# Performance work log

Hardware: AMD Instinct MI355X
Metric: run time of the kernel (lower is better)

## Reference

```python
import jax, jax.numpy as jnp
import numpy as np

V, SMAX, D, H, L, DFF, W = 32000, 1024, 1024, 16, 2, 4096, 256
HD = D // H
EPS = 1e-6


def setup_inputs() -> dict:
    key = jax.random.key(0)
    ks = jax.random.split(key, 20)
    s = lambda k, shape, scale=0.02: jax.random.normal(k, shape, dtype=jnp.float32) * scale
    return {
        "input_ids": jax.random.randint(ks[0], (2, SMAX), 0, V, dtype=jnp.int64),
        "emb": s(ks[1], (V, D)),
        "pos": s(ks[2], (SMAX, D)),
        "norm1_w": jnp.ones((L, D), jnp.float32),
        "norm2_w": jnp.ones((L, D), jnp.float32),
        "wq": s(ks[3], (L, D, D)), "bq": jnp.zeros((L, D), jnp.float32),
        "wk": s(ks[4], (L, D, D)), "bk": jnp.zeros((L, D), jnp.float32),
        "wv": s(ks[5], (L, D, D)), "bv": jnp.zeros((L, D), jnp.float32),
        "wo": s(ks[6], (L, D, D)), "bo": jnp.zeros((L, D), jnp.float32),
        "w1": s(ks[7], (L, D, DFF)), "b1": jnp.zeros((L, DFF), jnp.float32),
        "w2": s(ks[8], (L, DFF, D)), "b2": jnp.zeros((L, D), jnp.float32),
        "normf_w": jnp.ones((D,), jnp.float32),
    }


def rms(x, w):
    return x * jax.lax.rsqrt(jnp.mean(x * x, axis=-1, keepdims=True) + EPS) * w


def reference(input_ids, emb, pos, norm1_w, norm2_w, wq, bq, wk, bk, wv, bv,
              wo, bo, w1, b1, w2, b2, normf_w):
    B, S = input_ids.shape
    x = emb[input_ids] + pos[:S]  # [B,S,D]
    # sliding-window causal mask: attend to j with 0 <= i-j < W
    i = jnp.arange(S)[:, None]
    j = jnp.arange(S)[None, :]
    mask = (j <= i) & (i - j < W)  # [S,S]
    neg = jnp.asarray(-1e9, x.dtype)
    for l in range(L):
        h = rms(x, norm1_w[l])
        q = (h @ wq[l] + bq[l]).reshape(B, S, H, HD)
        k = (h @ wk[l] + bk[l]).reshape(B, S, H, HD)
        v = (h @ wv[l] + bv[l]).reshape(B, S, H, HD)
        scores = jnp.einsum('bqhd,bkhd->bhqk', q, k) / np.sqrt(HD).astype(np.float32)
        scores = jnp.where(mask[None, None], scores, neg)
        attn = jax.nn.softmax(scores, axis=-1)
        o = jnp.einsum('bhqk,bkhd->bqhd', attn, v).reshape(B, S, D)
        x = x + (o @ wo[l] + bo[l])
        h2 = rms(x, norm2_w[l])
        x = x + (jax.nn.gelu(h2 @ w1[l] + b1[l], approximate=False) @ w2[l] + b2[l])
    x = rms(x, normf_w)
    logits = x @ emb.T  # tied lm_head
    return logits
```

## Files before the change

### kernel.cpp

```cpp
#include <hip/hip_runtime.h>
#include <hip/hip_bf16.h>
#include <cstdint>

typedef __bf16 bf16;
typedef __bf16 bf16x8 __attribute__((ext_vector_type(8)));
typedef __bf16 bf16x4 __attribute__((ext_vector_type(4)));
typedef float  f32x4  __attribute__((ext_vector_type(4)));

constexpr int V_    = 32000;
constexpr int SMAX_ = 1024;
constexpr int D_    = 1024;
constexpr int H_    = 16;
constexpr int L_    = 2;
constexpr int DFF_  = 4096;
constexpr int WIN_  = 256;
constexpr int B_    = 2;
constexpr int M_    = B_ * SMAX_;

#define SBAR0_() __builtin_amdgcn_sched_barrier(0)
#define HWBAR_() { __builtin_amdgcn_s_barrier(); SBAR0_(); }
#define LGKM0_() { asm volatile("s_waitcnt lgkmcnt(0)" ::: "memory"); SBAR0_(); }
#define VM0_()   { asm volatile("s_waitcnt vmcnt(0)" ::: "memory"); SBAR0_(); }
#define VM8_()   { asm volatile("s_waitcnt vmcnt(8)" ::: "memory"); SBAR0_(); }

__global__ __launch_bounds__(512, 1) void gemm_lmA(
    const bf16* __restrict__ A, const bf16* __restrict__ BT,
    float* __restrict__ outf, int Nn)
{
  constexpr int KK = 1024, NT = KK / 32;
  __shared__ __align__(16) bf16 ldsA[4 * 8192];
  __shared__ __align__(16) bf16 ldsB[4 * 8192];

  const int t = threadIdx.x, lane = t & 63, w = t >> 6;
  const int l16 = lane & 15, lh = lane >> 4;
  const int wm = w >> 2, wn = w & 3;

  const int nloc = gridDim.x >> 3;
  const int wg = (blockIdx.x & 7) * nloc + (blockIdx.x >> 3);
  const long m0 = (long)(wg & 7) * 256;
  const long n0 = (long)(wg >> 3) * 256;

  auto STG = [&](const bf16* src, long rowBase, bf16* dst, int k0) {
    #pragma unroll
    for (int j = 0; j < 2; ++j) {
      int p = j * 8192 + t * 16;
      int row = p >> 6;
      int sl = ((p >> 4) & 3) ^ (row & 3);
      const bf16* g = src + (rowBase + row) * (long)KK + k0 + sl * 8;
      __builtin_amdgcn_global_load_lds(
          (const __attribute__((address_space(1))) uint32_t*)g,
          (__attribute__((address_space(3))) uint32_t*)(dst + j * 4096 + w * 512),
          16, 0, 0);
    }
  };
  auto LDF = [&](const bf16* base, int rowb) -> bf16x8 {
    int row = rowb + l16;
    return *(const bf16x8*)(base + row * 32 + ((lh ^ (l16 & 3)) << 3));
  };

  f32x4 acc[8][4] = {};

  STG(A, m0, ldsA,          0);  STG(BT, n0, ldsB,          0);
  STG(A, m0, ldsA + 8192,  32);  STG(BT, n0, ldsB + 8192,  32);
  STG(A, m0, ldsA + 16384, 64);  STG(BT, n0, ldsB + 16384, 64);
  int kNext = 96;

  for (int i = 0; i < NT; ++i) {
    const int cur = i & 3, nb = (i + 3) & 3;
    VM8_();
    HWBAR_();
    const bf16* Ac = ldsA + cur * 8192;
    const bf16* Bc = ldsB + cur * 8192;
    bf16x8 af[8], bb[4];
    #pragma unroll
    for (int mi = 0; mi < 8; ++mi) af[mi] = LDF(Ac, wm * 128 + mi * 16);
    #pragma unroll
    for (int ni = 0; ni < 4; ++ni) bb[ni] = LDF(Bc, wn * 64 + ni * 16);
    STG(A, m0, ldsA + nb * 8192, kNext);
    STG(BT, n0, ldsB + nb * 8192, kNext);
    kNext += 32; if (kNext == KK) kNext = 0;
    LGKM0_();
    __builtin_amdgcn_s_setprio(1);
    #pragma unroll
    for (int mi = 0; mi < 8; ++mi)
      #pragma unroll
      for (int ni = 0; ni < 4; ++ni)
        acc[mi][ni] = __builtin_amdgcn_mfma_f32_16x16x32_bf16(bb[ni], af[mi], acc[mi][ni], 0, 0, 0);
    __builtin_amdgcn_s_setprio(0);
  }

  asm volatile("s_waitcnt vmcnt(0) lgkmcnt(0)" ::: "memory");
  #pragma unroll
  for (int mi = 0; mi < 8; ++mi) {
    long row = m0 + wm * 128 + mi * 16 + l16;
    #pragma unroll
    for (int ni = 0; ni < 4; ++ni) {
      long col = n0 + wn * 64 + ni * 16 + lh * 4;
      *(f32x4*)(outf + row * Nn + col) = acc[mi][ni];
    }
  }
}

template<int BM, int EPI>
__global__ __launch_bounds__(256) void gemm_l2(
    const bf16* __restrict__ A, const bf16* __restrict__ BT,
    const float* __restrict__ bias, float* __restrict__ resid,
    bf16* __restrict__ outb, float* __restrict__ outf,
    int Nn, int Kk, int nbyMask, int nbyShift)
{
  constexpr int MR = BM / 32;
  constexpr int CA = BM / 32;
  __shared__ __align__(16) bf16 ldsA[2][BM * 64];
  __shared__ __align__(16) bf16 ldsB[2][8192];

  const int t = threadIdx.x, lane = t & 63, w = t >> 6;
  const int l16 = lane & 15, lh = lane >> 4;
  const int wm = w >> 1, wn = w & 1;

  const int nwg = gridDim.x, bid = blockIdx.x;
  const int nloc = nwg >> 3;
  const int wg = (bid & 7) * nloc + (bid >> 3);
  const long m0 = (long)(wg & nbyMask) * BM;
  const long n0 = (long)(wg >> nbyShift) * 128;

  auto STGA = [&](int c, int k0) {
    #pragma unroll
    for (int q = 0; q < CA; ++q) {
      int row = q * 32 + (t >> 3);
      int sl  = (t & 7) ^ (row & 7);
      const bf16* g = A + (m0 + row) * (long)Kk + k0 + sl * 8;
      __builtin_amdgcn_global_load_lds(
          (const __attribute__((address_space(1))) uint32_t*)g,
          (__attribute__((address_space(3))) uint32_t*)(&ldsA[c][q * 2048 + t * 8]),
          16, 0, 0);
    }
  };
  auto STGB = [&](int c, int k0) {
    #pragma unroll
    for (int q = 0; q < 4; ++q) {
      int row = q * 32 + (t >> 3);
      int sl  = (t & 7) ^ (row & 7);
      const bf16* g = BT + (n0 + row) * (long)Kk + k0 + sl * 8;
      __builtin_amdgcn_global_load_lds(
          (const __attribute__((address_space(1))) uint32_t*)g,
          (__attribute__((address_space(3))) uint32_t*)(&ldsB[c][q * 2048 + t * 8]),
          16, 0, 0);
    }
  };
  auto LDA = [&](int c, int mi, int ks) -> bf16x8 {
    int row = wm * (BM / 2) + mi * 16 + l16;
    int sl  = (ks * 4 + lh) ^ (row & 7);
    return *(const bf16x8*)(&ldsA[c][row * 64 + sl * 8]);
  };
  auto LDB = [&](int c, int ni, int ks) -> bf16x8 {
    int row = wn * 64 + ni * 16 + l16;
    int sl  = (ks * 4 + lh) ^ (row & 7);
    return *(const bf16x8*)(&ldsB[c][row * 64 + sl * 8]);
  };

  f32x4 acc[MR][4] = {};
  bf16x8 a[MR], b[4];

  STGA(0, 0); STGB(0, 0);
  int kNext = 64;

  const int NT = Kk >> 6;
  for (int j = 0; j < NT; ++j) {
    const int c = j & 1;
    VM0_();
    HWBAR_();
    #pragma unroll
    for (int mi = 0; mi < MR; ++mi) a[mi] = LDA(c, mi, 0);
    #pragma unroll
    for (int ni = 0; ni < 4; ++ni) b[ni] = LDB(c, ni, 0);
    STGA(c ^ 1, kNext); STGB(c ^ 1, kNext);
    LGKM0_();
    __builtin_amdgcn_s_setprio(1);
    #pragma unroll
    for (int mi = 0; mi < MR; ++mi)
      #pragma unroll
      for (int ni = 0; ni < 4; ++ni)
        acc[mi][ni] = __builtin_amdgcn_mfma_f32_16x16x32_bf16(b[ni], a[mi], acc[mi][ni], 0, 0, 0);
    __builtin_amdgcn_s_setprio(0);
    HWBAR_();
    #pragma unroll
    for (int mi = 0; mi < MR; ++mi) a[mi] = LDA(c, mi, 1);
    #pragma unroll
    for (int ni = 0; ni < 4; ++ni) b[ni] = LDB(c, ni, 1);
    LGKM0_();
    __builtin_amdgcn_s_setprio(1);
    #pragma unroll
    for (int mi = 0; mi < MR; ++mi)
      #pragma unroll
      for (int ni = 0; ni < 4; ++ni)
        acc[mi][ni] = __builtin_amdgcn_mfma_f32_16x16x32_bf16(b[ni], a[mi], acc[mi][ni], 0, 0, 0);
    __builtin_amdgcn_s_setprio(0);
    kNext += 64; if (kNext == Kk) kNext = 0;
  }

  #pragma unroll
  for (int mi = 0; mi < MR; ++mi) {
    long row = m0 + wm * (BM / 2) + mi * 16 + l16;
    #pragma unroll
    for (int ni = 0; ni < 4; ++ni) {
      long col = n0 + wn * 64 + ni * 16 + lh * 4;
      f32x4 v = acc[mi][ni];
      if (EPI == 3) {
        *(f32x4*)(outf + row * Nn + col) = v;
      } else {
        f32x4 bv = *(const f32x4*)(bias + col);
        v += bv;
        if (EPI == 0) {
          bf16x4 o;
          #pragma unroll
          for (int e = 0; e < 4; ++e) o[e] = (bf16)v[e];
          *(bf16x4*)(outb + row * Nn + col) = o;
        } else if (EPI == 1) {
          bf16x4 o;
          #pragma unroll
          for (int e = 0; e < 4; ++e) {
            float xx = v[e];
            o[e] = (bf16)(0.5f * xx * (1.0f + erff(xx * 0.70710678118654752f)));
          }
          *(bf16x4*)(outb + row * Nn + col) = o;
        } else {
          f32x4 r = *(f32x4*)(resid + row * Nn + col);
          r += v;
          *(f32x4*)(resid + row * Nn + col) = r;
        }
      }
    }
  }
}

__global__ __launch_bounds__(256) void attn_swa(
    const bf16* __restrict__ qkv, bf16* __restrict__ o)
{
  constexpr int PADK = 72;
  constexpr int PADV = 40;
  __shared__ bf16 Qs[64 * PADK];
  __shared__ bf16 Ks[32 * PADK];
  __shared__ bf16 Vt[64 * PADV];
  __shared__ bf16 Ps[4][16 * PADV];

  const int bid = blockIdx.x;
  const int qb = bid & 15;
  const int h  = (bid >> 4) & 15;
  const int b  = bid >> 8;
  const int q0 = qb * 64;
  const int t = threadIdx.x, lane = t & 63, w = t >> 6;
  const int l16 = lane & 15, lh = lane >> 4;

  #pragma unroll
  for (int i = 0; i < 2; i++) {
    int e = t + i * 256;
    int row = e >> 3, cc = e & 7;
    uint4 g = *(const uint4*)(qkv + ((long)(b * SMAX_ + q0 + row)) * 3072 + h * 64 + cc * 8);
    *(uint4*)(Qs + row * PADK + cc * 8) = g;
  }
  __syncthreads();
  bf16x8 aq[2];
  const int qrow = w * 16 + l16;
  #pragma unroll
  for (int ks = 0; ks < 2; ks++)
    aq[ks] = *(const bf16x8*)(Qs + qrow * PADK + ks * 32 + lh * 8);

  float m_run[4], l_run[4];
  f32x4 oacc[4];
  #pragma unroll
  for (int rr = 0; rr < 4; rr++) { m_run[rr] = -1e30f; l_run[rr] = 0.0f; }
  #pragma unroll
  for (int n = 0; n < 4; n++) oacc[n] = (f32x4){0.f, 0.f, 0.f, 0.f};

  const int tlo = q0 - (WIN_ - 1);
  const int jlo = (tlo <= 0) ? 0 : (tlo & ~31);
  const int iq  = q0 + w * 16 + lh * 4;

  for (int j0 = jlo; j0 < q0 + 64; j0 += 32) {
    __syncthreads();
    {
      int row = t >> 3, cc = t & 7;
      long base = ((long)(b * SMAX_ + j0 + row)) * 3072 + h * 64 + cc * 8;
      uint4 gk = *(const uint4*)(qkv + base + 1024);
      *(uint4*)(Ks + row * PADK + cc * 8) = gk;
      bf16x8 vv = *(const bf16x8*)(qkv + base + 2048);
      #pragma unroll
      for (int j = 0; j < 8; j++)
        Vt[(cc * 8 + j) * PADV + row] = vv[j];
    }
    __syncthreads();

    f32x4 s[2] = {(f32x4){0.f,0.f,0.f,0.f}, (f32x4){0.f,0.f,0.f,0.f}};
    #pragma unroll
    for (int nt = 0; nt < 2; nt++)
      #pragma unroll
      for (int ks = 0; ks < 2; ks++) {
        bf16x8 bk = *(const bf16x8*)(Ks + (nt * 16 + l16) * PADK + ks * 32 + lh * 8);
        s[nt] = __builtin_amdgcn_mfma_f32_16x16x32_bf16(aq[ks], bk, s[nt], 0, 0, 0);
      }

    float sc[2][4];
    #pragma unroll
    for (int nt = 0; nt < 2; nt++)
      #pragma unroll
      for (int rr = 0; rr < 4; rr++) {
        int i = iq + rr;
        int j = j0 + nt * 16 + l16;
        float v = s[nt][rr] * 0.125f;
        bool ok = (j <= i) && (i - j < WIN_);
        sc[nt][rr] = ok ? v : -1e30f;
      }

    float pb[2][4], alpha[4];
    #pragma unroll
    for (int rr = 0; rr < 4; rr++) {
      float mt = fmaxf(sc[0][rr], sc[1][rr]);
      #pragma unroll
      for (int off = 1; off < 16; off <<= 1) mt = fmaxf(mt, __shfl_xor(mt, off, 64));
      float mn = fmaxf(m_run[rr], mt);
      float a = __expf(m_run[rr] - mn);
      m_run[rr] = mn; alpha[rr] = a;
      float p0 = __expf(sc[0][rr] - mn);
      float p1 = __expf(sc[1][rr] - mn);
      pb[0][rr] = p0; pb[1][rr] = p1;
      float ls = p0 + p1;
      #pragma unroll
      for (int off = 1; off < 16; off <<= 1) ls += __shfl_xor(ls, off, 64);
      l_run[rr] = l_run[rr] * a + ls;
    }
    #pragma unroll
    for (int n = 0; n < 4; n++)
      #pragma unroll
      for (int rr = 0; rr < 4; rr++) oacc[n][rr] *= alpha[rr];

    #pragma unroll
    for (int rr = 0; rr < 4; rr++) {
      int prow = lh * 4 + rr;
      Ps[w][prow * PADV + l16]      = (bf16)pb[0][rr];
      Ps[w][prow * PADV + 16 + l16] = (bf16)pb[1][rr];
    }
    __syncthreads();

    bf16x8 pa = *(const bf16x8*)(&Ps[w][l16 * PADV + lh * 8]);
    #pragma unroll
    for (int n = 0; n < 4; n++) {
      bf16x8 bv = *(const bf16x8*)(Vt + (n * 16 + l16) * PADV + lh * 8);
      oacc[n] = __builtin_amdgcn_mfma_f32_16x16x32_bf16(pa, bv, oacc[n], 0, 0, 0);
    }
  }

  #pragma unroll
  for (int rr = 0; rr < 4; rr++) {
    int i = iq + rr;
    float inv = 1.0f / l_run[rr];
    #pragma unroll
    for (int n = 0; n < 4; n++)
      o[((long)(b * SMAX_ + i)) * D_ + h * 64 + n * 16 + l16] = (bf16)(oacc[n][rr] * inv);
  }
}

__global__ __launch_bounds__(256) void transpose_cvt(
    const float* __restrict__ src, bf16* __restrict__ dst,
    int Kk, int Nn, long srcL, long dstL)
{
  __shared__ float tile[32][33];
  const int tx = threadIdx.x, ty = threadIdx.y;
  const long n0 = (long)blockIdx.x * 32, k0 = (long)blockIdx.y * 32;
  src += (long)blockIdx.z * srcL;
  dst += (long)blockIdx.z * dstL;
  #pragma unroll
  for (int i = 0; i < 4; i++)
    tile[ty + i * 8][tx] = src[(k0 + ty + i * 8) * Nn + n0 + tx];
  __syncthreads();
  #pragma unroll
  for (int i = 0; i < 4; i++)
    dst[(n0 + ty + i * 8) * Kk + k0 + tx] = (bf16)tile[tx][ty + i * 8];
}

__global__ __launch_bounds__(256) void cvt_bf16(
    const float* __restrict__ src, bf16* __restrict__ dst, long n4)
{
  long i = (long)blockIdx.x * 256 + threadIdx.x;
  if (i >= n4) return;
  float4 v = ((const float4*)src)[i];
  bf16x4 o; o[0] = (bf16)v.x; o[1] = (bf16)v.y; o[2] = (bf16)v.z; o[3] = (bf16)v.w;
  ((bf16x4*)dst)[i] = o;
}

__global__ __launch_bounds__(256) void pack_bqkv(
    const float* __restrict__ bq, const float* __restrict__ bk,
    const float* __restrict__ bv, float* __restrict__ out)
{
  int i = blockIdx.x * 256 + threadIdx.x;
  if (i >= L_ * 3072) return;
  int l = i / 3072, c = i % 3072;
  float v = (c < 1024) ? bq[l * 1024 + c]
          : (c < 2048) ? bk[l * 1024 + c - 1024]
                       : bv[l * 1024 + c - 2048];
  out[i] = v;
}

__global__ __launch_bounds__(256) void embed_k(
    const int* __restrict__ ids, const float* __restrict__ emb,
    const float* __restrict__ pos, float* __restrict__ x)
{
  const int m = blockIdx.x, t = threadIdx.x;
  const int id = ids[m];
  const int s = m & (SMAX_ - 1);
  float4 e = ((const float4*)(emb + (long)id * D_))[t];
  float4 p = ((const float4*)(pos + (long)s * D_))[t];
  float4 rr; rr.x = e.x + p.x; rr.y = e.y + p.y; rr.z = e.z + p.z; rr.w = e.w + p.w;
  ((float4*)(x + (long)m * D_))[t] = rr;
}

__global__ __launch_bounds__(256) void rmsnorm_k(
    const float* __restrict__ x, const float* __restrict__ wgt,
    bf16* __restrict__ out)
{
  __shared__ float red[4];
  const int m = blockIdx.x, t = threadIdx.x;
  float4 v = ((const float4*)(x + (long)m * D_))[t];
  float ss = v.x * v.x + v.y * v.y + v.z * v.z + v.w * v.w;
  #pragma unroll
  for (int off = 1; off < 64; off <<= 1) ss += __shfl_xor(ss, off, 64);
  const int lane = t & 63, w = t >> 6;
  if (lane == 0) red[w] = ss;
  __syncthreads();
  float tot = red[0] + red[1] + red[2] + red[3];
  float rs = rsqrtf(tot * (1.0f / D_) + 1e-6f);
  float4 g = ((const float4*)wgt)[t];
  bf16x4 o;
  o[0] = (bf16)(v.x * rs * g.x); o[1] = (bf16)(v.y * rs * g.y);
  o[2] = (bf16)(v.z * rs * g.z); o[3] = (bf16)(v.w * rs * g.w);
  ((bf16x4*)(out + (long)m * D_))[t] = o;
}

extern "C" void kernel_launch(void* const* d_in, const int* in_sizes, int n_in,
                              void* d_out, int out_size, void* d_ws, size_t ws_size,
                              hipStream_t stream)
{
  const int*   ids = (const int*)d_in[0];
  const float* emb = (const float*)d_in[1];
  const float* pos = (const float*)d_in[2];
  const float* n1w = (const float*)d_in[3];
  const float* n2w = (const float*)d_in[4];
  const float* wq  = (const float*)d_in[5];
  const float* bq  = (const float*)d_in[6];
  const float* wk  = (const float*)d_in[7];
  const float* bk  = (const float*)d_in[8];
  const float* wv  = (const float*)d_in[9];
  const float* bv  = (const float*)d_in[10];
  const float* wo  = (const float*)d_in[11];
  const float* bo  = (const float*)d_in[12];
  const float* w1  = (const float*)d_in[13];
  const float* b1  = (const float*)d_in[14];
  const float* w2  = (const float*)d_in[15];
  const float* b2  = (const float*)d_in[16];
  const float* nfw = (const float*)d_in[17];

  char* p = (char*)d_ws;
  auto alloc = [&](size_t bytes) {
    char* rr = p; p += (bytes + 255) & ~(size_t)255; return rr;
  };
  bf16*  wqkv_t = (bf16*) alloc((size_t)L_ * 3 * 1024 * 1024 * 2);
  bf16*  wo_t   = (bf16*) alloc((size_t)L_ * 1024 * 1024 * 2);
  bf16*  w1_t   = (bf16*) alloc((size_t)L_ * 4096 * 1024 * 2);
  bf16*  w2_t   = (bf16*) alloc((size_t)L_ * 1024 * 4096 * 2);
  bf16*  emb_bf = (bf16*) alloc((size_t)V_ * D_ * 2);
  float* bqkv   = (float*)alloc((size_t)L_ * 3072 * 4);
  float* x      = (float*)alloc((size_t)M_ * D_ * 4);
  bf16*  hbuf   = (bf16*) alloc((size_t)M_ * D_ * 2);
  bf16*  qkv    = (bf16*) alloc((size_t)M_ * 3072 * 2);
  bf16*  obuf   = (bf16*) alloc((size_t)M_ * D_ * 2);
  bf16*  ff     = (bf16*) alloc((size_t)M_ * DFF_ * 2);

  const dim3 b32(32, 8, 1);
  transpose_cvt<<<dim3(32, 32, L_),  b32, 0, stream>>>(wq, wqkv_t,                1024, 1024, 1024 * 1024, 3 * 1024 * 1024);
  transpose_cvt<<<dim3(32, 32, L_),  b32, 0, stream>>>(wk, wqkv_t + 1024 * 1024,  1024, 1024, 1024 * 1024, 3 * 1024 * 1024);
  transpose_cvt<<<dim3(32, 32, L_),  b32, 0, stream>>>(wv, wqkv_t + 2*1024*1024,  1024, 1024, 1024 * 1024, 3 * 1024 * 1024);
  transpose_cvt<<<dim3(32, 32, L_),  b32, 0, stream>>>(wo, wo_t,                  1024, 1024, 1024 * 1024, 1024 * 1024);
  transpose_cvt<<<dim3(128, 32, L_), b32, 0, stream>>>(w1, w1_t,                  1024, 4096, 1024 * 4096, 4096 * 1024);
  transpose_cvt<<<dim3(32, 128, L_), b32, 0, stream>>>(w2, w2_t,                  4096, 1024, 4096 * 1024, 1024 * 4096);
  cvt_bf16<<<32000, 256, 0, stream>>>(emb, emb_bf, (long)V_ * D_ / 4);
  pack_bqkv<<<24, 256, 0, stream>>>(bq, bk, bv, bqkv);
  embed_k<<<M_, 256, 0, stream>>>(ids, emb, pos, x);

  for (int l = 0; l < L_; l++) {
    rmsnorm_k<<<M_, 256, 0, stream>>>(x, n1w + l * D_, hbuf);
    gemm_l2<64, 0><<<dim3(32 * 24), 256, 0, stream>>>(
        hbuf, wqkv_t + (size_t)l * 3 * 1024 * 1024, bqkv + l * 3072,
        nullptr, qkv, nullptr, 3072, 1024, 31, 5);
    attn_swa<<<B_ * H_ * (SMAX_ / 64), 256, 0, stream>>>(qkv, obuf);
    gemm_l2<64, 2><<<dim3(32 * 8), 256, 0, stream>>>(
        obuf, wo_t + (size_t)l * 1024 * 1024, bo + l * D_,
        x, nullptr, nullptr, 1024, 1024, 31, 5);
    rmsnorm_k<<<M_, 256, 0, stream>>>(x, n2w + l * D_, hbuf);
    gemm_l2<128, 1><<<dim3(16 * 32), 256, 0, stream>>>(
        hbuf, w1_t + (size_t)l * 4096 * 1024, b1 + l * DFF_,
        nullptr, ff, nullptr, 4096, 1024, 15, 4);
    gemm_l2<64, 2><<<dim3(32 * 8), 256, 0, stream>>>(
        ff, w2_t + (size_t)l * 1024 * 4096, b2 + l * D_,
        x, nullptr, nullptr, 1024, 4096, 31, 5);
  }
  rmsnorm_k<<<M_, 256, 0, stream>>>(x, nfw, hbuf);
  gemm_lmA<<<dim3(8 * (V_ / 256)), 512, 0, stream>>>(
      hbuf, emb_bf, (float*)d_out, V_);
}
```

Before: 620.6 us.

## Piggyback weight transposes and embedding conversion onto layer-0 kernels as extra blocks

Removes the standalone transpose, convert and bias-pack launches. Their work becomes extra trailing blocks appended to the layer-0 rmsnorm, GEMM and attention launches. Each piece is scheduled one launch ahead of its first consumer, so stream ordering still guarantees correctness. The aim is to fill idle CUs during small or tail-bound kernels and cut launch overhead. In exchange, each host kernel reserves its own LDS footprint for the aux blocks, and the main kernels may be slowed by bandwidth contention.

Result: faster. 558.6 us (-10.0%).

```diff
diff --git a/kernel.cpp b/kernel.cpp
--- a/kernel.cpp
+++ b/kernel.cpp
@@ -23,6 +23,65 @@
 #define VM0_()   { asm volatile("s_waitcnt vmcnt(0)" ::: "memory"); SBAR0_(); }
 #define VM8_()   { asm volatile("s_waitcnt vmcnt(8)" ::: "memory"); SBAR0_(); }
 
+struct AuxArgs {
+  const float *wq, *wk, *wv, *wo, *w1, *w2, *emb, *bq, *bk, *bv;
+  bf16 *wqkv_t, *wo_t, *w1_t, *w2_t, *emb_bf;
+  float *bqkv;
+  int kind;
+  int base;
+};
+
+__device__ __forceinline__ void aux_transpose(
+    const float* src, bf16* dst, int Kk, int Nn, int tid, int t)
+{
+  __shared__ float tile[32][33];
+  const int tx = t & 31, ty = t >> 5;
+  int tilesX = Nn >> 5;
+  int n0 = (tid % tilesX) << 5, k0 = (tid / tilesX) << 5;
+  #pragma unroll
+  for (int i = 0; i < 4; i++)
+    tile[ty + i * 8][tx] = src[(long)(k0 + ty + i * 8) * Nn + n0 + tx];
+  __syncthreads();
+  #pragma unroll
+  for (int i = 0; i < 4; i++)
+    dst[(long)(n0 + ty + i * 8) * Kk + k0 + tx] = (bf16)tile[tx][ty + i * 8];
+}
+
+__device__ __forceinline__ void aux_do(const AuxArgs& A, int b, int t)
+{
+  if (A.kind == 0) {
+    if (b < 8192) {
+      int mat = b >> 11, r = b & 2047, z = r >> 10, tid = r & 1023;
+      const float* s; bf16* d;
+      if (mat == 0)      { s = A.wq + (long)z * 1048576; d = A.wqkv_t + (long)z * 3145728; }
+      else if (mat == 1) { s = A.wk + (long)z * 1048576; d = A.wqkv_t + (long)z * 3145728 + 1048576; }
+      else if (mat == 2) { s = A.wv + (long)z * 1048576; d = A.wqkv_t + (long)z * 3145728 + 2097152; }
+      else               { s = A.wo + (long)z * 1048576; d = A.wo_t   + (long)z * 1048576; }
+      aux_transpose(s, d, 1024, 1024, tid, t);
+    } else {
+      int i = (b - 8192) * 256 + t;
+      if (i < L_ * 3072) {
+        int l = i / 3072, c = i % 3072;
+        float v = (c < 1024) ? A.bq[l * 1024 + c]
+                : (c < 2048) ? A.bk[l * 1024 + c - 1024]
+                             : A.bv[l * 1024 + c - 2048];
+        A.bqkv[i] = v;
+      }
+    }
+  } else if (A.kind == 1) {
+    int z = b >> 12, tid = b & 4095;
+    aux_transpose(A.w1 + (long)z * 4194304, A.w1_t + (long)z * 4194304, 1024, 4096, tid, t);
+  } else if (A.kind == 2) {
+    int z = b >> 12, tid = b & 4095;
+    aux_transpose(A.w2 + (long)z * 4194304, A.w2_t + (long)z * 4194304, 4096, 1024, tid, t);
+  } else if (A.kind == 3) {
+    long i = (long)(A.base + b) * 256 + t;
+    float4 v = ((const float4*)A.emb)[i];
+    bf16x4 o; o[0] = (bf16)v.x; o[1] = (bf16)v.y; o[2] = (bf16)v.z; o[3] = (bf16)v.w;
+    ((bf16x4*)A.emb_bf)[i] = o;
+  }
+}
+
 __global__ __launch_bounds__(512, 1) void gemm_lmA(
     const bf16* __restrict__ A, const bf16* __restrict__ BT,
     float* __restrict__ outf, int Nn)
@@ -106,8 +165,13 @@
     const bf16* __restrict__ A, const bf16* __restrict__ BT,
     const float* __restrict__ bias, float* __restrict__ resid,
     bf16* __restrict__ outb, float* __restrict__ outf,
-    int Nn, int Kk, int nbyMask, int nbyShift)
-{
+    int Nn, int Kk, int nbyMask, int nbyShift,
+    AuxArgs aux, int mainBlocks)
+{
+  if ((int)blockIdx.x >= mainBlocks) {
+    aux_do(aux, (int)blockIdx.x - mainBlocks, threadIdx.x);
+    return;
+  }
   constexpr int MR = BM / 32;
   constexpr int CA = BM / 32;
   __shared__ __align__(16) bf16 ldsA[2][BM * 64];
@@ -117,7 +181,7 @@
   const int l16 = lane & 15, lh = lane >> 4;
   const int wm = w >> 1, wn = w & 1;
 
-  const int nwg = gridDim.x, bid = blockIdx.x;
+  const int nwg = mainBlocks, bid = blockIdx.x;
   const int nloc = nwg >> 3;
   const int wg = (bid & 7) * nloc + (bid >> 3);
   const long m0 = (long)(wg & nbyMask) * BM;
@@ -234,8 +298,13 @@
 }
 
 __global__ __launch_bounds__(256) void attn_swa(
-    const bf16* __restrict__ qkv, bf16* __restrict__ o)
-{
+    const bf16* __restrict__ qkv, bf16* __restrict__ o,
+    AuxArgs aux, int mainBlocks)
+{
+  if ((int)blockIdx.x >= mainBlocks) {
+    aux_do(aux, (int)blockIdx.x - mainBlocks, threadIdx.x);
+    return;
+  }
   constexpr int PADK = 72;
   constexpr int PADV = 40;
   __shared__ bf16 Qs[64 * PADK];
@@ -359,47 +428,6 @@
   }
 }
 
-__global__ __launch_bounds__(256) void transpose_cvt(
-    const float* __restrict__ src, bf16* __restrict__ dst,
-    int Kk, int Nn, long srcL, long dstL)
-{
-  __shared__ float tile[32][33];
-  const int tx = threadIdx.x, ty = threadIdx.y;
-  const long n0 = (long)blockIdx.x * 32, k0 = (long)blockIdx.y * 32;
-  src += (long)blockIdx.z * srcL;
-  dst += (long)blockIdx.z * dstL;
-  #pragma unroll
-  for (int i = 0; i < 4; i++)
-    tile[ty + i * 8][tx] = src[(k0 + ty + i * 8) * Nn + n0 + tx];
-  __syncthreads();
-  #pragma unroll
-  for (int i = 0; i < 4; i++)
-    dst[(n0 + ty + i * 8) * Kk + k0 + tx] = (bf16)tile[tx][ty + i * 8];
-}
-
-__global__ __launch_bounds__(256) void cvt_bf16(
-    const float* __restrict__ src, bf16* __restrict__ dst, long n4)
-{
-  long i = (long)blockIdx.x * 256 + threadIdx.x;
-  if (i >= n4) return;
-  float4 v = ((const float4*)src)[i];
-  bf16x4 o; o[0] = (bf16)v.x; o[1] = (bf16)v.y; o[2] = (bf16)v.z; o[3] = (bf16)v.w;
-  ((bf16x4*)dst)[i] = o;
-}
-
-__global__ __launch_bounds__(256) void pack_bqkv(
-    const float* __restrict__ bq, const float* __restrict__ bk,
-    const float* __restrict__ bv, float* __restrict__ out)
-{
-  int i = blockIdx.x * 256 + threadIdx.x;
-  if (i >= L_ * 3072) return;
-  int l = i / 3072, c = i % 3072;
-  float v = (c < 1024) ? bq[l * 1024 + c]
-          : (c < 2048) ? bk[l * 1024 + c - 1024]
-                       : bv[l * 1024 + c - 2048];
-  out[i] = v;
-}
-
 __global__ __launch_bounds__(256) void embed_k(
     const int* __restrict__ ids, const float* __restrict__ emb,
     const float* __restrict__ pos, float* __restrict__ x)
@@ -415,8 +443,12 @@
 
 __global__ __launch_bounds__(256) void rmsnorm_k(
     const float* __restrict__ x, const float* __restrict__ wgt,
-    bf16* __restrict__ out)
-{
+    bf16* __restrict__ out, AuxArgs aux, int mainBlocks)
+{
+  if ((int)blockIdx.x >= mainBlocks) {
+    aux_do(aux, (int)blockIdx.x - mainBlocks, threadIdx.x);
+    return;
+  }
   __shared__ float red[4];
   const int m = blockIdx.x, t = threadIdx.x;
   float4 v = ((const float4*)(x + (long)m * D_))[t];
@@ -474,35 +506,55 @@
   bf16*  obuf   = (bf16*) alloc((size_t)M_ * D_ * 2);
   bf16*  ff     = (bf16*) alloc((size_t)M_ * DFF_ * 2);
 
-  const dim3 b32(32, 8, 1);
-  transpose_cvt<<<dim3(32, 32, L_),  b32, 0, stream>>>(wq, wqkv_t,                1024, 1024, 1024 * 1024, 3 * 1024 * 1024);
-  transpose_cvt<<<dim3(32, 32, L_),  b32, 0, stream>>>(wk, wqkv_t + 1024 * 1024,  1024, 1024, 1024 * 1024, 3 * 1024 * 1024);
-  transpose_cvt<<<dim3(32, 32, L_),  b32, 0, stream>>>(wv, wqkv_t + 2*1024*1024,  1024, 1024, 1024 * 1024, 3 * 1024 * 1024);
-  transpose_cvt<<<dim3(32, 32, L_),  b32, 0, stream>>>(wo, wo_t,                  1024, 1024, 1024 * 1024, 1024 * 1024);
-  transpose_cvt<<<dim3(128, 32, L_), b32, 0, stream>>>(w1, w1_t,                  1024, 4096, 1024 * 4096, 4096 * 1024);
-  transpose_cvt<<<dim3(32, 128, L_), b32, 0, stream>>>(w2, w2_t,                  4096, 1024, 4096 * 1024, 1024 * 4096);
-  cvt_bf16<<<32000, 256, 0, stream>>>(emb, emb_bf, (long)V_ * D_ / 4);
-  pack_bqkv<<<24, 256, 0, stream>>>(bq, bk, bv, bqkv);
+  auto mk = [&](int kind, int base) {
+    AuxArgs a;
+    a.wq = wq; a.wk = wk; a.wv = wv; a.wo = wo; a.w1 = w1; a.w2 = w2;
+    a.emb = emb; a.bq = bq; a.bk = bk; a.bv = bv;
+    a.wqkv_t = wqkv_t; a.wo_t = wo_t; a.w1_t = w1_t; a.w2_t = w2_t;
+    a.emb_bf = emb_bf; a.bqkv = bqkv;
+    a.kind = kind; a.base = base;
+    return a;
+  };
+  AuxArgs auxNone = mk(-1, 0);
+
   embed_k<<<M_, 256, 0, stream>>>(ids, emb, pos, x);
 
   for (int l = 0; l < L_; l++) {
-    rmsnorm_k<<<M_, 256, 0, stream>>>(x, n1w + l * D_, hbuf);
-    gemm_l2<64, 0><<<dim3(32 * 24), 256, 0, stream>>>(
-        hbuf, wqkv_t + (size_t)l * 3 * 1024 * 1024, bqkv + l * 3072,
-        nullptr, qkv, nullptr, 3072, 1024, 31, 5);
-    attn_swa<<<B_ * H_ * (SMAX_ / 64), 256, 0, stream>>>(qkv, obuf);
-    gemm_l2<64, 2><<<dim3(32 * 8), 256, 0, stream>>>(
-        obuf, wo_t + (size_t)l * 1024 * 1024, bo + l * D_,
-        x, nullptr, nullptr, 1024, 1024, 31, 5);
-    rmsnorm_k<<<M_, 256, 0, stream>>>(x, n2w + l * D_, hbuf);
-    gemm_l2<128, 1><<<dim3(16 * 32), 256, 0, stream>>>(
-        hbuf, w1_t + (size_t)l * 4096 * 1024, b1 + l * DFF_,
-        nullptr, ff, nullptr, 4096, 1024, 15, 4);
-    gemm_l2<64, 2><<<dim3(32 * 8), 256, 0, stream>>>(
-        ff, w2_t + (size_t)l * 1024 * 4096, b2 + l * D_,
-        x, nullptr, nullptr, 1024, 4096, 31, 5);
-  }
-  rmsnorm_k<<<M_, 256, 0, stream>>>(x, nfw, hbuf);
+    if (l == 0) {
+      rmsnorm_k<<<2048 + 8216, 256, 0, stream>>>(x, n1w, hbuf, mk(0, 0), 2048);
+      gemm_l2<64, 0><<<768 + 8192, 256, 0, stream>>>(
+          hbuf, wqkv_t, bqkv, nullptr, qkv, nullptr,
+          3072, 1024, 31, 5, mk(1, 0), 768);
+      attn_swa<<<512 + 10667, 256, 0, stream>>>(qkv, obuf, mk(3, 0), 512);
+      gemm_l2<64, 2><<<256 + 10667, 256, 0, stream>>>(
+          obuf, wo_t, bo, x, nullptr, nullptr,
+          1024, 1024, 31, 5, mk(3, 10667), 256);
+      rmsnorm_k<<<2048 + 8192, 256, 0, stream>>>(x, n2w, hbuf, mk(2, 0), 2048);
+      gemm_l2<128, 1><<<512, 256, 0, stream>>>(
+          hbuf, w1_t, b1, nullptr, ff, nullptr,
+          4096, 1024, 15, 4, auxNone, 512);
+      gemm_l2<64, 2><<<256 + 10666, 256, 0, stream>>>(
+          ff, w2_t, b2, x, nullptr, nullptr,
+          1024, 4096, 31, 5, mk(3, 21334), 256);
+    } else {
+      rmsnorm_k<<<2048, 256, 0, stream>>>(x, n1w + l * D_, hbuf, auxNone, 2048);
+      gemm_l2<64, 0><<<768, 256, 0, stream>>>(
+          hbuf, wqkv_t + (size_t)l * 3 * 1024 * 1024, bqkv + l * 3072,
+          nullptr, qkv, nullptr, 3072, 1024, 31, 5, auxNone, 768);
+      attn_swa<<<512, 256, 0, stream>>>(qkv, obuf, auxNone, 512);
+      gemm_l2<64, 2><<<256, 256, 0, stream>>>(
+          obuf, wo_t + (size_t)l * 1024 * 1024, bo + l * D_,
+          x, nullptr, nullptr, 1024, 1024, 31, 5, auxNone, 256);
+      rmsnorm_k<<<2048, 256, 0, stream>>>(x, n2w + l * D_, hbuf, auxNone, 2048);
+      gemm_l2<128, 1><<<512, 256, 0, stream>>>(
+          hbuf, w1_t + (size_t)l * 4096 * 1024, b1 + l * DFF_,
+          nullptr, ff, nullptr, 4096, 1024, 15, 4, auxNone, 512);
+      gemm_l2<64, 2><<<256, 256, 0, stream>>>(
+          ff, w2_t + (size_t)l * 1024 * 4096, b2 + l * D_,
+          x, nullptr, nullptr, 1024, 4096, 31, 5, auxNone, 256);
+    }
+  }
+  rmsnorm_k<<<2048, 256, 0, stream>>>(x, nfw, hbuf, auxNone, 2048);
   gemm_lmA<<<dim3(8 * (V_ / 256)), 512, 0, stream>>>(
       hbuf, emb_bf, (float*)d_out, V_);
 }
```
